# Kernel tuning notes

Hardware: AMD Instinct MI355X
Metric: run time of the kernel (lower is better)

## Reference

```python
import jax, jax.numpy as jnp
import numpy as np

PI = 3.141592653589793
M = 1500.0; IZ = 2250.0; LF = 1.2; LR = 1.6; CF = 80000.0; CR = 80000.0
TAU_A = 0.1; TAU_DELTA = 0.1
MAX_STEER = 30.0 * PI / 180.0
MAX_ACCEL = 3.0; MIN_ACCEL = -6.0
MU = 0.9; G = 9.81
L = LF + LR
FY_F_MAX = MU * M * G * (LR / L)
FY_R_MAX = MU * M * G * (LF / L)
V_EFF_MIN = 20.0 / 3.6
DT = 0.1
DT_INT = 0.01
B = 4194304


def setup_inputs() -> dict:
    key = jax.random.key(0)
    k1, k2 = jax.random.split(key)
    init_state = jax.random.normal(k1, (B, 9), dtype=jnp.float32)
    action = jax.random.normal(k2, (B, 2), dtype=jnp.float32)
    return {"init_state": init_state, "action": action}


def _substep(state, a_ref, h):
    # state: (B, 9) = [x, y, psi, v, a, delta, beta, r, delta_ref]
    x, y, psi, v, a, delta, beta, r, delta_ref = (state[:, i] for i in range(9))
    a_dot = (a_ref - a) / TAU_A
    delta_dot = (delta_ref - delta) / TAU_DELTA
    v_eff = jnp.maximum(v, V_EFF_MIN)
    alpha_f = beta + LF * r / v_eff - delta
    alpha_r = beta - LR * r / v_eff
    F_yf = jnp.clip(-CF * alpha_f, -FY_F_MAX, FY_F_MAX)
    F_yr = jnp.clip(-CR * alpha_r, -FY_R_MAX, FY_R_MAX)
    beta_dot = (F_yf + F_yr) / (M * v_eff) - r
    r_dot = (LF * F_yf - LR * F_yr) / IZ
    psi_eff = psi + beta
    new_state = jnp.stack([
        x + v * jnp.cos(psi_eff) * h,
        y + v * jnp.sin(psi_eff) * h,
        psi + r * h,
        jnp.maximum(v + a * h, 0.0),
        a + a_dot * h,
        jnp.clip(delta + delta_dot * h, -MAX_STEER, MAX_STEER),
        beta + beta_dot * h,
        r + r_dot * h,
        delta_ref,
    ], axis=1)
    return new_state


def _forward(init_state, action):
    # reset(): postprocess clamps
    s = init_state
    s = s.at[:, 3].set(jnp.maximum(s[:, 3], 0.0))
    s = s.at[:, 5].set(jnp.clip(s[:, 5], -MAX_STEER, MAX_STEER))
    s = s.at[:, 8].set(jnp.clip(s[:, 8], -MAX_STEER, MAX_STEER))
    # step(): ZOH action, clamp, overwrite delta_ref
    a_ref = jnp.clip(action[:, 0], MIN_ACCEL, MAX_ACCEL)
    delta_ref_cmd = jnp.clip(action[:, 1], -MAX_STEER, MAX_STEER)
    s = s.at[:, 8].set(delta_ref_cmd)
    # replicate torch's Python float substep bookkeeping exactly
    n_full = int(DT // DT_INT)
    dt_rem = DT - n_full * DT_INT
    h = jnp.float32(DT_INT)

    def body(st, _):
        return _substep(st, a_ref, h), None

    s, _ = jax.lax.scan(body, s, None, length=n_full)
    if dt_rem > 1e-12:
        s = _substep(s, a_ref, jnp.float32(dt_rem))
    return s


def reference(init_state, action):
    return _forward(init_state, action)
```

## Files before the change

kernel.cpp:

```cpp
#include <hip/hip_runtime.h>
#include <math.h>


typedef float v2f __attribute__((ext_vector_type(2)));
typedef float f4  __attribute__((ext_vector_type(4)));

__device__ __forceinline__ float med3(float x, float lo, float hi) {
    return __builtin_amdgcn_fmed3f(x, lo, hi);
}
__device__ __forceinline__ v2f vfma2(v2f a, v2f b, v2f c) {
    return __builtin_elementwise_fma(a, b, c);
}

__global__ __launch_bounds__(256) void bicycle_kernel(
    const float* __restrict__ state_in,
    const float* __restrict__ action_in,
    float* __restrict__ out)
{
    constexpr float MAX_STEER = (float)(30.0 * 3.141592653589793 / 180.0);
    constexpr float V_EFF_MIN = (float)(20.0 / 3.6);
    constexpr float FY_F_MAX  = (float)(0.9 * 1500.0 * 9.81 * (1.6 / 2.8));
    constexpr float FY_R_MAX  = (float)(0.9 * 1500.0 * 9.81 * (1.2 / 2.8));

    __shared__ float smem[4 * 2304];

    const int tid  = threadIdx.x;
    const int wid  = tid >> 6;
    const int lane = tid & 63;
    const size_t waveRow = (size_t)blockIdx.x * 1024 + (size_t)wid * 256;

    float* ws  = smem + wid * 2304;
    f4*    ws4 = (f4*)ws;

    const f4* g4 = (const f4*)(state_in + waveRow * 9);
    f4 rg[9];
#pragma unroll
    for (int i = 0; i < 9; ++i) rg[i] = g4[lane + 64 * i];

    const float2* a2 = (const float2*)action_in + waveRow;
    float2 act[4];
#pragma unroll
    for (int j = 0; j < 4; ++j) act[j] = a2[lane + 64 * j];

#pragma unroll
    for (int i = 0; i < 9; ++i) ws4[lane + 64 * i] = rg[i];
    asm volatile("s_waitcnt lgkmcnt(0)" ::: "memory");

    v2f x[2], y[2], psi[2], v[2], a[2], delta[2], beta[2], r[2];
    v2f a_ref[2], d_ref[2], cs[2], sn[2];
#pragma unroll
    for (int p = 0; p < 2; ++p) {
        const int r0 = (lane + 64 * (2 * p + 0)) * 9;
        const int r1 = (lane + 64 * (2 * p + 1)) * 9;
        x[p]     = (v2f){ws[r0 + 0], ws[r1 + 0]};
        y[p]     = (v2f){ws[r0 + 1], ws[r1 + 1]};
        psi[p]   = (v2f){ws[r0 + 2], ws[r1 + 2]};
        v[p]     = (v2f){fmaxf(ws[r0 + 3], 0.0f), fmaxf(ws[r1 + 3], 0.0f)};
        a[p]     = (v2f){ws[r0 + 4], ws[r1 + 4]};
        delta[p] = (v2f){med3(ws[r0 + 5], -MAX_STEER, MAX_STEER),
                         med3(ws[r1 + 5], -MAX_STEER, MAX_STEER)};
        beta[p]  = (v2f){ws[r0 + 6], ws[r1 + 6]};
        r[p]     = (v2f){ws[r0 + 7], ws[r1 + 7]};
        a_ref[p] = (v2f){med3(act[2 * p + 0].x, -6.0f, 3.0f),
                         med3(act[2 * p + 1].x, -6.0f, 3.0f)};
        d_ref[p] = (v2f){med3(act[2 * p + 0].y, -MAX_STEER, MAX_STEER),
                         med3(act[2 * p + 1].y, -MAX_STEER, MAX_STEER)};
        float s0, c0, s1, c1;
        __sincosf(psi[p].x + beta[p].x, &s0, &c0);
        __sincosf(psi[p].y + beta[p].y, &s1, &c1);
        cs[p] = (v2f){c0, c1};
        sn[p] = (v2f){s0, s1};
    }

#pragma unroll
    for (int k = 0; k < 10; ++k) {
#pragma unroll
        for (int p = 0; p < 2; ++p) {
            v2f v_eff = {fmaxf(v[p].x, V_EFF_MIN), fmaxf(v[p].y, V_EFF_MIN)};
            v2f inv_v = {__builtin_amdgcn_rcpf(v_eff.x), __builtin_amdgcn_rcpf(v_eff.y)};
            v2f t = r[p] * inv_v;
            v2f alpha_f = vfma2((v2f)(1.2f), t, beta[p]) - delta[p];
            v2f alpha_r = vfma2((v2f)(-1.6f), t, beta[p]);
            v2f Ff_raw = alpha_f * -80000.0f;
            v2f Fr_raw = alpha_r * -80000.0f;
            v2f F_yf = {med3(Ff_raw.x, -FY_F_MAX, FY_F_MAX), med3(Ff_raw.y, -FY_F_MAX, FY_F_MAX)};
            v2f F_yr = {med3(Fr_raw.x, -FY_R_MAX, FY_R_MAX), med3(Fr_raw.y, -FY_R_MAX, FY_R_MAX)};
            v2f beta_dot = vfma2(F_yf + F_yr, inv_v * (1.0f / 1500.0f), -r[p]);
            v2f r_dot = vfma2((v2f)(1.2f), F_yf, F_yr * -1.6f) * (1.0f / 2250.0f);

            v2f vh = v[p] * 0.01f;
            x[p] = vfma2(vh, cs[p], x[p]);
            y[p] = vfma2(vh, sn[p], y[p]);

            v2f d  = (r[p] + beta_dot) * 0.01f;
            v2f cd = vfma2(d * d, (v2f)(-0.5f), (v2f)(1.0f));
            v2f cs_n = vfma2(cs[p], cd, -(sn[p] * d));
            v2f sn_n = vfma2(sn[p], cd, cs[p] * d);

            v2f v_new = vfma2(a[p], (v2f)(0.01f), v[p]);
            v_new = (v2f){fmaxf(v_new.x, 0.0f), fmaxf(v_new.y, 0.0f)};
            psi[p]  = vfma2(r[p], (v2f)(0.01f), psi[p]);
            a[p]    = vfma2(a_ref[p] - a[p], (v2f)(0.1f), a[p]);
            v2f dlt = vfma2(d_ref[p] - delta[p], (v2f)(0.1f), delta[p]);
            delta[p] = (v2f){med3(dlt.x, -MAX_STEER, MAX_STEER), med3(dlt.y, -MAX_STEER, MAX_STEER)};
            beta[p] = vfma2(beta_dot, (v2f)(0.01f), beta[p]);
            r[p]    = vfma2(r_dot, (v2f)(0.01f), r[p]);
            v[p] = v_new;
            cs[p] = cs_n;
            sn[p] = sn_n;
        }
    }

#pragma unroll
    for (int p = 0; p < 2; ++p) {
        const int r0 = (lane + 64 * (2 * p + 0)) * 9;
        const int r1 = (lane + 64 * (2 * p + 1)) * 9;
        ws[r0 + 0] = x[p].x;     ws[r1 + 0] = x[p].y;
        ws[r0 + 1] = y[p].x;     ws[r1 + 1] = y[p].y;
        ws[r0 + 2] = psi[p].x;   ws[r1 + 2] = psi[p].y;
        ws[r0 + 3] = v[p].x;     ws[r1 + 3] = v[p].y;
        ws[r0 + 4] = a[p].x;     ws[r1 + 4] = a[p].y;
        ws[r0 + 5] = delta[p].x; ws[r1 + 5] = delta[p].y;
        ws[r0 + 6] = beta[p].x;  ws[r1 + 6] = beta[p].y;
        ws[r0 + 7] = r[p].x;     ws[r1 + 7] = r[p].y;
        ws[r0 + 8] = d_ref[p].x; ws[r1 + 8] = d_ref[p].y;
    }
    asm volatile("s_waitcnt lgkmcnt(0)" ::: "memory");

    f4* o4 = (f4*)(out + waveRow * 9);
#pragma unroll
    for (int i = 0; i < 9; ++i)
        __builtin_nontemporal_store(ws4[lane + 64 * i], &o4[lane + 64 * i]);
}

extern "C" void kernel_launch(void* const* d_in, const int* in_sizes, int n_in,
                              void* d_out, int out_size, void* d_ws, size_t ws_size,
                              hipStream_t stream) {
    const float* state  = (const float*)d_in[0];
    const float* action = (const float*)d_in[1];
    float* out = (float*)d_out;
    const int rows = in_sizes[0] / 9;
    const int grid = rows / 1024;
    bicycle_kernel<<<grid, 256, 0, stream>>>(state, action, out);
}
```

Before: 57.13 us.

## Process four row tiles per wave with software-pipelined prefetch of next tile

Each wave now handles four 256-row tiles in sequence. It issues the global loads for the next tile into registers before computing the current one, so memory latency overlaps with compute. The grid shrinks by a factor of four and launch bounds request 4 blocks per CU. The extra prefetch registers may raise register pressure, and the smaller grid reduces parallelism for hiding latency across waves.

Measured after the change: 56.08 us. No clear change (-1.8%).

```diff
diff --git a/kernel.cpp b/kernel.cpp
--- a/kernel.cpp
+++ b/kernel.cpp
@@ -12,7 +12,7 @@
     return __builtin_elementwise_fma(a, b, c);
 }
 
-__global__ __launch_bounds__(256) void bicycle_kernel(
+__global__ __launch_bounds__(256, 4) void bicycle_kernel(
     const float* __restrict__ state_in,
     const float* __restrict__ action_in,
     float* __restrict__ out)
@@ -27,110 +27,129 @@
     const int tid  = threadIdx.x;
     const int wid  = tid >> 6;
     const int lane = tid & 63;
-    const size_t waveRow = (size_t)blockIdx.x * 1024 + (size_t)wid * 256;
-
     float* ws  = smem + wid * 2304;
     f4*    ws4 = (f4*)ws;
 
-    const f4* g4 = (const f4*)(state_in + waveRow * 9);
-    f4 rg[9];
+    const size_t W = (size_t)blockIdx.x * 4 + wid;
+
+    f4     pk[9];
+    float2 actp[4];
+
+    auto loadp = [&](int t) {
+        const size_t R = (W * 4 + (size_t)t) * 256;
+        const f4* g4 = (const f4*)(state_in + R * 9);
 #pragma unroll
-    for (int i = 0; i < 9; ++i) rg[i] = g4[lane + 64 * i];
+        for (int i = 0; i < 9; ++i) pk[i] = g4[lane + 64 * i];
+        const float2* a2 = (const float2*)action_in + R;
+#pragma unroll
+        for (int j = 0; j < 4; ++j) actp[j] = a2[lane + 64 * j];
+    };
+    auto commit = [&]() {
+#pragma unroll
+        for (int i = 0; i < 9; ++i) ws4[lane + 64 * i] = pk[i];
+    };
 
-    const float2* a2 = (const float2*)action_in + waveRow;
-    float2 act[4];
-#pragma unroll
-    for (int j = 0; j < 4; ++j) act[j] = a2[lane + 64 * j];
+    loadp(0);
+    commit();
 
 #pragma unroll
-    for (int i = 0; i < 9; ++i) ws4[lane + 64 * i] = rg[i];
-    asm volatile("s_waitcnt lgkmcnt(0)" ::: "memory");
+    for (int t = 0; t < 4; ++t) {
+        v2f a_ref[2], d_ref[2];
+#pragma unroll
+        for (int p = 0; p < 2; ++p) {
+            a_ref[p] = (v2f){med3(actp[2 * p + 0].x, -6.0f, 3.0f),
+                             med3(actp[2 * p + 1].x, -6.0f, 3.0f)};
+            d_ref[p] = (v2f){med3(actp[2 * p + 0].y, -MAX_STEER, MAX_STEER),
+                             med3(actp[2 * p + 1].y, -MAX_STEER, MAX_STEER)};
+        }
+        if (t < 3) loadp(t + 1);
 
-    v2f x[2], y[2], psi[2], v[2], a[2], delta[2], beta[2], r[2];
-    v2f a_ref[2], d_ref[2], cs[2], sn[2];
+        v2f x[2], y[2], psi[2], v[2], a[2], delta[2], beta[2], r[2], cs[2], sn[2];
 #pragma unroll
-    for (int p = 0; p < 2; ++p) {
-        const int r0 = (lane + 64 * (2 * p + 0)) * 9;
-        const int r1 = (lane + 64 * (2 * p + 1)) * 9;
-        x[p]     = (v2f){ws[r0 + 0], ws[r1 + 0]};
-        y[p]     = (v2f){ws[r0 + 1], ws[r1 + 1]};
-        psi[p]   = (v2f){ws[r0 + 2], ws[r1 + 2]};
-        v[p]     = (v2f){fmaxf(ws[r0 + 3], 0.0f), fmaxf(ws[r1 + 3], 0.0f)};
-        a[p]     = (v2f){ws[r0 + 4], ws[r1 + 4]};
-        delta[p] = (v2f){med3(ws[r0 + 5], -MAX_STEER, MAX_STEER),
-                         med3(ws[r1 + 5], -MAX_STEER, MAX_STEER)};
-        beta[p]  = (v2f){ws[r0 + 6], ws[r1 + 6]};
-        r[p]     = (v2f){ws[r0 + 7], ws[r1 + 7]};
-        a_ref[p] = (v2f){med3(act[2 * p + 0].x, -6.0f, 3.0f),
-                         med3(act[2 * p + 1].x, -6.0f, 3.0f)};
-        d_ref[p] = (v2f){med3(act[2 * p + 0].y, -MAX_STEER, MAX_STEER),
-                         med3(act[2 * p + 1].y, -MAX_STEER, MAX_STEER)};
-        float s0, c0, s1, c1;
-        __sincosf(psi[p].x + beta[p].x, &s0, &c0);
-        __sincosf(psi[p].y + beta[p].y, &s1, &c1);
-        cs[p] = (v2f){c0, c1};
-        sn[p] = (v2f){s0, s1};
-    }
+        for (int p = 0; p < 2; ++p) {
+            const int r0 = (lane + 64 * (2 * p + 0)) * 9;
+            const int r1 = (lane + 64 * (2 * p + 1)) * 9;
+            x[p]     = (v2f){ws[r0 + 0], ws[r1 + 0]};
+            y[p]     = (v2f){ws[r0 + 1], ws[r1 + 1]};
+            psi[p]   = (v2f){ws[r0 + 2], ws[r1 + 2]};
+            v[p]     = (v2f){fmaxf(ws[r0 + 3], 0.0f), fmaxf(ws[r1 + 3], 0.0f)};
+            a[p]     = (v2f){ws[r0 + 4], ws[r1 + 4]};
+            delta[p] = (v2f){med3(ws[r0 + 5], -MAX_STEER, MAX_STEER),
+                             med3(ws[r1 + 5], -MAX_STEER, MAX_STEER)};
+            beta[p]  = (v2f){ws[r0 + 6], ws[r1 + 6]};
+            r[p]     = (v2f){ws[r0 + 7], ws[r1 + 7]};
+            float s0, c0, s1, c1;
+            __sincosf(psi[p].x + beta[p].x, &s0, &c0);
+            __sincosf(psi[p].y + beta[p].y, &s1, &c1);
+            cs[p] = (v2f){c0, c1};
+            sn[p] = (v2f){s0, s1};
+        }
 
 #pragma unroll
-    for (int k = 0; k < 10; ++k) {
+        for (int k = 0; k < 10; ++k) {
+#pragma unroll
+            for (int p = 0; p < 2; ++p) {
+                v2f v_eff = {fmaxf(v[p].x, V_EFF_MIN), fmaxf(v[p].y, V_EFF_MIN)};
+                v2f inv_v = {__builtin_amdgcn_rcpf(v_eff.x), __builtin_amdgcn_rcpf(v_eff.y)};
+                v2f tt = r[p] * inv_v;
+                v2f alpha_f = vfma2((v2f)(1.2f), tt, beta[p]) - delta[p];
+                v2f alpha_r = vfma2((v2f)(-1.6f), tt, beta[p]);
+                v2f Ff_raw = alpha_f * -80000.0f;
+                v2f Fr_raw = alpha_r * -80000.0f;
+                v2f F_yf = {med3(Ff_raw.x, -FY_F_MAX, FY_F_MAX), med3(Ff_raw.y, -FY_F_MAX, FY_F_MAX)};
+                v2f F_yr = {med3(Fr_raw.x, -FY_R_MAX, FY_R_MAX), med3(Fr_raw.y, -FY_R_MAX, FY_R_MAX)};
+                v2f beta_dot = vfma2(F_yf + F_yr, inv_v * (1.0f / 1500.0f), -r[p]);
+                v2f r_dot = vfma2((v2f)(1.2f), F_yf, F_yr * -1.6f) * (1.0f / 2250.0f);
+
+                v2f vh = v[p] * 0.01f;
+                x[p] = vfma2(vh, cs[p], x[p]);
+                y[p] = vfma2(vh, sn[p], y[p]);
+
+                v2f d  = (r[p] + beta_dot) * 0.01f;
+                v2f cd = vfma2(d * d, (v2f)(-0.5f), (v2f)(1.0f));
+                v2f cs_n = vfma2(cs[p], cd, -(sn[p] * d));
+                v2f sn_n = vfma2(sn[p], cd, cs[p] * d);
+
+                v2f v_new = vfma2(a[p], (v2f)(0.01f), v[p]);
+                v_new = (v2f){fmaxf(v_new.x, 0.0f), fmaxf(v_new.y, 0.0f)};
+                psi[p]  = vfma2(r[p], (v2f)(0.01f), psi[p]);
+                a[p]    = vfma2(a_ref[p] - a[p], (v2f)(0.1f), a[p]);
+                v2f dlt = vfma2(d_ref[p] - delta[p], (v2f)(0.1f), delta[p]);
+                delta[p] = (v2f){med3(dlt.x, -MAX_STEER, MAX_STEER), med3(dlt.y, -MAX_STEER, MAX_STEER)};
+                beta[p] = vfma2(beta_dot, (v2f)(0.01f), beta[p]);
+                r[p]    = vfma2(r_dot, (v2f)(0.01f), r[p]);
+                v[p] = v_new;
+                cs[p] = cs_n;
+                sn[p] = sn_n;
+            }
+        }
+
 #pragma unroll
         for (int p = 0; p < 2; ++p) {
-            v2f v_eff = {fmaxf(v[p].x, V_EFF_MIN), fmaxf(v[p].y, V_EFF_MIN)};
-            v2f inv_v = {__builtin_amdgcn_rcpf(v_eff.x), __builtin_amdgcn_rcpf(v_eff.y)};
-            v2f t = r[p] * inv_v;
-            v2f alpha_f = vfma2((v2f)(1.2f), t, beta[p]) - delta[p];
-            v2f alpha_r = vfma2((v2f)(-1.6f), t, beta[p]);
-            v2f Ff_raw = alpha_f * -80000.0f;
-            v2f Fr_raw = alpha_r * -80000.0f;
-            v2f F_yf = {med3(Ff_raw.x, -FY_F_MAX, FY_F_MAX), med3(Ff_raw.y, -FY_F_MAX, FY_F_MAX)};
-            v2f F_yr = {med3(Fr_raw.x, -FY_R_MAX, FY_R_MAX), med3(Fr_raw.y, -FY_R_MAX, FY_R_MAX)};
-            v2f beta_dot = vfma2(F_yf + F_yr, inv_v * (1.0f / 1500.0f), -r[p]);
-            v2f r_dot = vfma2((v2f)(1.2f), F_yf, F_yr * -1.6f) * (1.0f / 2250.0f);
+            const int r0 = (lane + 64 * (2 * p + 0)) * 9;
+            const int r1 = (lane + 64 * (2 * p + 1)) * 9;
+            ws[r0 + 0] = x[p].x;     ws[r1 + 0] = x[p].y;
+            ws[r0 + 1] = y[p].x;     ws[r1 + 1] = y[p].y;
+            ws[r0 + 2] = psi[p].x;   ws[r1 + 2] = psi[p].y;
+            ws[r0 + 3] = v[p].x;     ws[r1 + 3] = v[p].y;
+            ws[r0 + 4] = a[p].x;     ws[r1 + 4] = a[p].y;
+            ws[r0 + 5] = delta[p].x; ws[r1 + 5] = delta[p].y;
+            ws[r0 + 6] = beta[p].x;  ws[r1 + 6] = beta[p].y;
+            ws[r0 + 7] = r[p].x;     ws[r1 + 7] = r[p].y;
+            ws[r0 + 8] = d_ref[p].x; ws[r1 + 8] = d_ref[p].y;
+        }
 
-            v2f vh = v[p] * 0.01f;
-            x[p] = vfma2(vh, cs[p], x[p]);
-            y[p] = vfma2(vh, sn[p], y[p]);
+        f4 st[9];
+#pragma unroll
+        for (int i = 0; i < 9; ++i) st[i] = ws4[lane + 64 * i];
+        const size_t R = (W * 4 + (size_t)t) * 256;
+        f4* o4 = (f4*)(out + R * 9);
+#pragma unroll
+        for (int i = 0; i < 9; ++i)
+            __builtin_nontemporal_store(st[i], &o4[lane + 64 * i]);
 
-            v2f d  = (r[p] + beta_dot) * 0.01f;
-            v2f cd = vfma2(d * d, (v2f)(-0.5f), (v2f)(1.0f));
-            v2f cs_n = vfma2(cs[p], cd, -(sn[p] * d));
-            v2f sn_n = vfma2(sn[p], cd, cs[p] * d);
-
-            v2f v_new = vfma2(a[p], (v2f)(0.01f), v[p]);
-            v_new = (v2f){fmaxf(v_new.x, 0.0f), fmaxf(v_new.y, 0.0f)};
-            psi[p]  = vfma2(r[p], (v2f)(0.01f), psi[p]);
-            a[p]    = vfma2(a_ref[p] - a[p], (v2f)(0.1f), a[p]);
-            v2f dlt = vfma2(d_ref[p] - delta[p], (v2f)(0.1f), delta[p]);
-            delta[p] = (v2f){med3(dlt.x, -MAX_STEER, MAX_STEER), med3(dlt.y, -MAX_STEER, MAX_STEER)};
-            beta[p] = vfma2(beta_dot, (v2f)(0.01f), beta[p]);
-            r[p]    = vfma2(r_dot, (v2f)(0.01f), r[p]);
-            v[p] = v_new;
-            cs[p] = cs_n;
-            sn[p] = sn_n;
-        }
+        if (t < 3) commit();
     }
-
-#pragma unroll
-    for (int p = 0; p < 2; ++p) {
-        const int r0 = (lane + 64 * (2 * p + 0)) * 9;
-        const int r1 = (lane + 64 * (2 * p + 1)) * 9;
-        ws[r0 + 0] = x[p].x;     ws[r1 + 0] = x[p].y;
-        ws[r0 + 1] = y[p].x;     ws[r1 + 1] = y[p].y;
-        ws[r0 + 2] = psi[p].x;   ws[r1 + 2] = psi[p].y;
-        ws[r0 + 3] = v[p].x;     ws[r1 + 3] = v[p].y;
-        ws[r0 + 4] = a[p].x;     ws[r1 + 4] = a[p].y;
-        ws[r0 + 5] = delta[p].x; ws[r1 + 5] = delta[p].y;
-        ws[r0 + 6] = beta[p].x;  ws[r1 + 6] = beta[p].y;
-        ws[r0 + 7] = r[p].x;     ws[r1 + 7] = r[p].y;
-        ws[r0 + 8] = d_ref[p].x; ws[r1 + 8] = d_ref[p].y;
-    }
-    asm volatile("s_waitcnt lgkmcnt(0)" ::: "memory");
-
-    f4* o4 = (f4*)(out + waveRow * 9);
-#pragma unroll
-    for (int i = 0; i < 9; ++i)
-        __builtin_nontemporal_store(ws4[lane + 64 * i], &o4[lane + 64 * i]);
 }
 
 extern "C" void kernel_launch(void* const* d_in, const int* in_sizes, int n_in,
@@ -140,6 +159,6 @@
     const float* action = (const float*)d_in[1];
     float* out = (float*)d_out;
     const int rows = in_sizes[0] / 9;
-    const int grid = rows / 1024;
+    const int grid = rows / 4096;
     bicycle_kernel<<<grid, 256, 0, stream>>>(state, action, out);
 }
```
